# Optimization experiments

Hardware: AMD Instinct MI355X
Metric: run time of the kernel (lower is better)

Reference implementation:

```python
import jax, jax.numpy as jnp
import numpy as np

EPS_DIST = 1e-7  # matches torch: log((d+1)/(d+1e-7))


def _cdist(x, p):
    # x: (B, N, D), p: (P, D) -> (B, N, P) Euclidean distances
    x2 = jnp.sum(x * x, axis=-1, keepdims=True)        # (B, N, 1)
    p2 = jnp.sum(p * p, axis=-1)                       # (P,)
    d2 = x2 + p2[None, None, :] - 2.0 * jnp.einsum('bnd,pd->bnp', x, p)
    return jnp.sqrt(jnp.maximum(d2, 1e-12))


def setup_inputs() -> dict:
    key = jax.random.key(0)
    k1, k2, k3 = jax.random.split(key, 3)
    B, C, H, W = 32, 2048, 14, 14
    num_classes, npc = 200, 10
    P = num_classes * npc
    x = jax.random.normal(k1, (B, C, H, W), dtype=jnp.float32)
    prototypes = jax.random.normal(k2, (1, P, C), dtype=jnp.float32)
    fc_w = jax.random.normal(k3, (num_classes, P), dtype=jnp.float32) * 0.02
    return {"x": x, "prototypes": prototypes, "fc_w": fc_w}


def reference(x, prototypes, fc_w):
    B, C, H, W = x.shape
    feats = x.reshape(B, C, H * W).transpose(0, 2, 1)   # (B, HW, D)
    protos = prototypes[0]                              # (P, D)
    num_classes = fc_w.shape[0]
    npc = protos.shape[0] // num_classes

    distances = _cdist(feats, protos)                   # (B, HW, P)
    similarity = jnp.log((distances + 1.0) / (distances + EPS_DIST))
    max_similarity = jnp.max(similarity, axis=1)        # (B, P)
    min_distances = jnp.min(distances, axis=1)          # (B, P)
    min_distances_per_class = min_distances.reshape(B, num_classes, npc)
    scores = max_similarity @ fc_w.T                    # (B, num_classes)
    return scores, min_distances_per_class
```

## Files before the change

### kernel.cpp

```cpp
#include <hip/hip_runtime.h>

#define INF_BITS 0x7F800000u
#define AS1 __attribute__((address_space(1)))
#define AS3 __attribute__((address_space(3)))

typedef float f32x4 __attribute__((ext_vector_type(4)));
typedef __bf16 bf16x8 __attribute__((ext_vector_type(8)));
typedef unsigned short u16x4 __attribute__((ext_vector_type(4)));
typedef unsigned short u16x8 __attribute__((ext_vector_type(8)));
typedef unsigned int u32x4 __attribute__((ext_vector_type(4)));

static __device__ __forceinline__ unsigned short f2bf(float f) {
  unsigned int u = __float_as_uint(f);
  return (unsigned short)((u + 0x7FFFu + ((u >> 16) & 1u)) >> 16);
}

__global__ __launch_bounds__(256) void k_prep_p(const float* __restrict__ protos,
                                                unsigned short* __restrict__ pT,
                                                float* __restrict__ p2,
                                                unsigned int* __restrict__ outu) {
  const int row = blockIdx.x;
  const int tid = threadIdx.x;
  const int gi = row * 256 + tid;
  if (gi < 64000) outu[6400 + gi] = INF_BITS;
  __shared__ float red[4];
  float s = 0.f;
  u16x8 h = (u16x8){0, 0, 0, 0, 0, 0, 0, 0};
  if (row < 2000) {
    const float* src = protos + (size_t)row * 2048 + tid * 8;
    f32x4 a = *(const f32x4*)src;
    f32x4 c = *(const f32x4*)(src + 4);
    h = (u16x8){f2bf(a.x), f2bf(a.y), f2bf(a.z), f2bf(a.w),
                f2bf(c.x), f2bf(c.y), f2bf(c.z), f2bf(c.w)};
    s = a.x * a.x + a.y * a.y + a.z * a.z + a.w * a.w +
        c.x * c.x + c.y * c.y + c.z * c.z + c.w * c.w;
  }
  *(u16x8*)(pT + (size_t)row * 2048 + tid * 8) = h;
  #pragma unroll
  for (int off = 32; off; off >>= 1) s += __shfl_xor(s, off);
  if ((tid & 63) == 0) red[tid >> 6] = s;
  __syncthreads();
  if (tid == 0) p2[row] = red[0] + red[1] + red[2] + red[3];
}

__global__ __launch_bounds__(256) void k_prep_x(const float* __restrict__ x,
                                                unsigned short* __restrict__ xT,
                                                float* __restrict__ x2p,
                                                float* __restrict__ x2) {
  const int kt = blockIdx.x;
  const int b  = blockIdx.y;
  const int tid = threadIdx.x;
  if (b == 32) {
    u32x4* pad = (u32x4*)(xT + (size_t)6272 * 2048);
    #pragma unroll
    for (int j = tid; j < 1024; j += 256)
      pad[kt * 1024 + j] = (u32x4){0u, 0u, 0u, 0u};
    if (kt == 0 && tid < 128) x2[6272 + tid] = __uint_as_float(INF_BITS);
    return;
  }
  __shared__ unsigned short Ls[64][204];
  const float* src = x + ((size_t)b * 2048 + (size_t)kt * 64) * 196;
  for (int idx = tid; idx < 3136; idx += 256) {
    const int kk = idx / 49, c4 = idx - kk * 49;
    f32x4 v = *(const f32x4*)(src + (size_t)kk * 196 + c4 * 4);
    *(u16x4*)&Ls[kk][c4 * 4] = (u16x4){f2bf(v.x), f2bf(v.y), f2bf(v.z), f2bf(v.w)};
  }
  __syncthreads();
  if (tid < 196) {
    float s = 0.f;
    #pragma unroll
    for (int j = 0; j < 64; ++j) {
      float v = __uint_as_float((unsigned int)Ls[j][tid] << 16);
      s += v * v;
    }
    x2p[kt * 6272 + b * 196 + tid] = s;
  }
  unsigned short* dstb = xT + (size_t)b * 196 * 2048 + kt * 64;
  for (int idx = tid; idx < 1568; idx += 256) {
    const int n = idx >> 3, q = idx & 7;
    const int k0 = q * 8;
    u32x4 v;
    v.x = (unsigned int)Ls[k0 + 0][n] | ((unsigned int)Ls[k0 + 1][n] << 16);
    v.y = (unsigned int)Ls[k0 + 2][n] | ((unsigned int)Ls[k0 + 3][n] << 16);
    v.z = (unsigned int)Ls[k0 + 4][n] | ((unsigned int)Ls[k0 + 5][n] << 16);
    v.w = (unsigned int)Ls[k0 + 6][n] | ((unsigned int)Ls[k0 + 7][n] << 16);
    *(u32x4*)(dstb + (size_t)n * 2048 + k0) = v;
  }
}

__global__ void k_x2r(const float* __restrict__ x2p, float* __restrict__ x2) {
  int i = blockIdx.x * blockDim.x + threadIdx.x;
  if (i >= 6272) return;
  float s = 0.f;
  #pragma unroll
  for (int c = 0; c < 32; ++c) s += x2p[c * 6272 + i];
  x2[i] = s;
}

__global__ __launch_bounds__(512, 2) void k_main(
    const unsigned short* __restrict__ pT, const unsigned short* __restrict__ xT,
    const float* __restrict__ p2, const float* __restrict__ x2,
    unsigned int* __restrict__ outu) {
  const int orig = blockIdx.x;
  const int wgid = (orig & 7) * 25 + (orig >> 3);
  const int ptpair = wgid / 50;
  const int rem = wgid - ptpair * 50;
  const int ptile = ptpair * 2 + (rem & 1);
  const int mtile = rem >> 1;
  const int p0 = ptile * 256;
  const int m0 = mtile * 256;
  const int tid = threadIdx.x;
  const int lane = tid & 63;
  const int w = tid >> 6;
  const int wp = w >> 2;
  const int wn = w & 3;
  const int lr = lane & 15;
  const int lg = lane >> 4;

  __shared__ __align__(16) char S[131072];

  f32x4 acc[8][4];
  #pragma unroll
  for (int mi = 0; mi < 8; ++mi)
    #pragma unroll
    for (int ni = 0; ni < 4; ++ni)
      acc[mi][ni] = (f32x4){0.f, 0.f, 0.f, 0.f};

  const int rowbase = tid >> 3;
  const int chunk = (tid & 7) ^ (rowbase & 7);
  const char* gA = (const char*)pT + (size_t)(p0 + rowbase) * 4096 + chunk * 16;
  const char* gB = (const char*)xT + (size_t)(m0 + rowbase) * 4096 + chunk * 16;
  const int wbase = w * 1024;

#define STAGE_A(c_, kt_, h_) do {                                              \
    const char* s_ = gA + (size_t)((h_) * 128 * 4096) + (size_t)(kt_) * 128;   \
    _Pragma("unroll")                                                          \
    for (int j_ = 0; j_ < 2; ++j_)                                             \
      __builtin_amdgcn_global_load_lds(                                        \
          (const AS1 void*)(s_ + (size_t)j_ * 64 * 4096),                      \
          (AS3 void*)(S + (c_) * 32768 + (h_) * 16384 + j_ * 8192 + wbase),    \
          16, 0, 0);                                                           \
  } while (0)
#define STAGE_B(c_, kt_, h_) do {                                              \
    const char* s_ = gB + (size_t)((h_) * 128 * 4096) + (size_t)(kt_) * 128;   \
    _Pragma("unroll")                                                          \
    for (int j_ = 0; j_ < 2; ++j_)                                             \
      __builtin_amdgcn_global_load_lds(                                        \
          (const AS1 void*)(s_ + (size_t)j_ * 64 * 4096),                      \
          (AS3 void*)(S + 65536 + (c_) * 32768 + (h_) * 16384 + j_ * 8192 + wbase), \
          16, 0, 0);                                                           \
  } while (0)

  const int swz = ((lr & 7) << 4);
  const int arow = (wp * 128 + lr) * 128;
  const int brow = (wn * 64 + lr) * 128;
  const int koff0 = (lg * 16) ^ swz;
  const int koff1 = (64 + lg * 16) ^ swz;

#define READ_A(dst_, c_, ko_, hf_)                                             \
    _Pragma("unroll")                                                          \
    for (int mi_ = 0; mi_ < 4; ++mi_)                                          \
      dst_[mi_] = *(const bf16x8*)(S + (c_) * 32768 + arow + (hf_) * 8192 +    \
                                   mi_ * 2048 + (ko_));
#define READ_B(dst_, c_, ko_)                                                  \
    _Pragma("unroll")                                                          \
    for (int ni_ = 0; ni_ < 4; ++ni_)                                          \
      dst_[ni_] = *(const bf16x8*)(S + 65536 + (c_) * 32768 + brow +           \
                                   ni_ * 2048 + (ko_));

#define PH_BAR() do { __builtin_amdgcn_sched_barrier(0);                       \
    __builtin_amdgcn_s_barrier(); __builtin_amdgcn_sched_barrier(0); } while (0)
#define LGKM0() do { asm volatile("s_waitcnt lgkmcnt(0)" ::: "memory");        \
    __builtin_amdgcn_sched_barrier(0); } while (0)
#define MFMA_Q(mlo_, af_, bf_) do { __builtin_amdgcn_s_setprio(1);             \
    _Pragma("unroll")                                                          \
    for (int mi_ = (mlo_); mi_ < (mlo_) + 4; ++mi_)                            \
      _Pragma("unroll")                                                        \
      for (int ni_ = 0; ni_ < 4; ++ni_)                                        \
        acc[mi_][ni_] = __builtin_amdgcn_mfma_f32_16x16x32_bf16(               \
            af_[mi_ - (mlo_)], bf_[ni_], acc[mi_][ni_], 0, 0, 0);              \
    __builtin_amdgcn_s_setprio(0); } while (0)

#define KT_BODY(kt_, c_, sa_, sb_, vm_) do {                                   \
    bf16x8 alo[4], ahi[4], bk0[4], bk1[4];                                     \
    READ_A(alo, c_, koff0, 0);                                                 \
    READ_B(bk0, c_, koff0);                                                    \
    if (sa_) STAGE_A((c_) ^ 1, (kt_) + 1, 0);                                  \
    PH_BAR(); LGKM0();                                                         \
    MFMA_Q(0, alo, bk0);                                                       \
    PH_BAR();                                                                  \
    READ_A(ahi, c_, koff0, 1);                                                 \
    READ_B(bk1, c_, koff1);                                                    \
    if (sa_) STAGE_A((c_) ^ 1, (kt_) + 1, 1);                                  \
    PH_BAR(); LGKM0();                                                         \
    MFMA_Q(4, ahi, bk0);                                                       \
    PH_BAR();                                                                  \
    READ_A(alo, c_, koff1, 0);                                                 \
    if (sb_) STAGE_B(c_, (kt_) + 2, 0);                                        \
    PH_BAR(); LGKM0();                                                         \
    MFMA_Q(0, alo, bk1);                                                       \
    PH_BAR();                                                                  \
    READ_A(ahi, c_, koff1, 1);                                                 \
    if (sb_) STAGE_B(c_, (kt_) + 2, 1);                                        \
    if ((vm_) == 4)      asm volatile("s_waitcnt vmcnt(4)" ::: "memory");      \
    else if ((vm_) == 0) asm volatile("s_waitcnt vmcnt(0)" ::: "memory");      \
    __builtin_amdgcn_sched_barrier(0);                                         \
    PH_BAR(); LGKM0();                                                         \
    MFMA_Q(4, ahi, bk1);                                                       \
    PH_BAR();                                                                  \
  } while (0)

  STAGE_B(0, 0, 0); STAGE_B(0, 0, 1);
  STAGE_A(0, 0, 0); STAGE_A(0, 0, 1);
  STAGE_B(1, 1, 0); STAGE_B(1, 1, 1);
  asm volatile("s_waitcnt vmcnt(4)" ::: "memory");
  __builtin_amdgcn_sched_barrier(0);
  __builtin_amdgcn_s_barrier();
  __builtin_amdgcn_sched_barrier(0);

  #pragma unroll 1
  for (int it = 0; it < 15; ++it) {
    KT_BODY(2 * it, 0, 1, 1, 4);
    KT_BODY(2 * it + 1, 1, 1, 1, 4);
  }
  KT_BODY(30, 0, 1, 0, 0);
  KT_BODY(31, 1, 0, 0, -1);
#undef KT_BODY
#undef MFMA_Q
#undef READ_A
#undef READ_B
#undef STAGE_A
#undef STAGE_B

  const int wm_base = m0 + wn * 64;
  const int b_lo = wm_base / 196;
  int b_hi = (wm_base + 63) / 196;
  if (b_hi > 31) b_hi = 31;
  const bool wave_ok = (b_lo < 32);
  float x2v[4];
  int seg0[4];
  #pragma unroll
  for (int ni = 0; ni < 4; ++ni) {
    const int m = wm_base + ni * 16 + lr;
    x2v[ni] = x2[m];
    seg0[ni] = ((m / 196) == b_lo);
  }
  const float INF = __uint_as_float(INF_BITS);
  #pragma unroll
  for (int mi = 0; mi < 8; ++mi) {
    const int prow = p0 + wp * 128 + mi * 16 + 4 * lg;
    #pragma unroll
    for (int j = 0; j < 4; ++j) {
      const int p = prow + j;
      const float pp = p2[p];
      float ma = INF, mb = INF;
      #pragma unroll
      for (int ni = 0; ni < 4; ++ni) {
        const float d2 = x2v[ni] + pp - 2.f * acc[mi][ni][j];
        ma = fminf(ma, seg0[ni] ? d2 : INF);
        mb = fminf(mb, seg0[ni] ? INF : d2);
      }
      #pragma unroll
      for (int off = 1; off < 16; off <<= 1) {
        ma = fminf(ma, __shfl_xor(ma, off));
        mb = fminf(mb, __shfl_xor(mb, off));
      }
      if (lr == 0 && p < 2000 && wave_ok) {
        atomicMin(&outu[6400 + b_lo * 2000 + p], __float_as_uint(fmaxf(ma, 0.f)));
        if (b_hi != b_lo)
          atomicMin(&outu[6400 + b_hi * 2000 + p], __float_as_uint(fmaxf(mb, 0.f)));
      }
    }
  }
}

__global__ void k_post(float* __restrict__ out, float* __restrict__ simbuf) {
  int i = blockIdx.x * blockDim.x + threadIdx.x;
  if (i >= 64000) return;
  float d2 = out[6400 + i];
  float d = sqrtf(fmaxf(d2, 1e-12f));
  out[6400 + i] = d;
  simbuf[i] = logf((d + 1.0f) / (d + 1e-7f));
}

__global__ __launch_bounds__(256) void k_scores(const float* __restrict__ fc_w,
                                                const float* __restrict__ simbuf,
                                                float* __restrict__ out) {
  const int id = blockIdx.x * 4 + (threadIdx.x >> 6);
  const int lane = threadIdx.x & 63;
  const int b = id / 200;
  const int c = id - b * 200;
  const f32x4* sv = (const f32x4*)(simbuf + (size_t)b * 2000);
  const f32x4* wv = (const f32x4*)(fc_w + (size_t)c * 2000);
  float s = 0.f;
  #pragma unroll
  for (int it = 0; it < 8; ++it) {
    int i = lane + it * 64;
    if (i < 500) {
      f32x4 a = sv[i], w4 = wv[i];
      s += a.x * w4.x + a.y * w4.y + a.z * w4.z + a.w * w4.w;
    }
  }
  #pragma unroll
  for (int off = 32; off; off >>= 1) s += __shfl_xor(s, off);
  if (lane == 0) out[b * 200 + c] = s;
}

extern "C" void kernel_launch(void* const* d_in, const int* in_sizes, int n_in,
                              void* d_out, int out_size, void* d_ws, size_t ws_size,
                              hipStream_t stream) {
  const float* x      = (const float*)d_in[0];
  const float* protos = (const float*)d_in[1];
  const float* fc_w   = (const float*)d_in[2];
  float* out = (float*)d_out;

  char* wsb = (char*)d_ws;
  unsigned short* pT = (unsigned short*)wsb;
  unsigned short* xT = (unsigned short*)(wsb + 8388608);
  float* p2   = (float*)(wsb + 34603008);
  float* x2   = (float*)(wsb + 34611200);
  float* x2p  = (float*)(wsb + 34636800);
  float* simb = (float*)(wsb + 34636800);

  k_prep_p<<<2048, 256, 0, stream>>>(protos, pT, p2, (unsigned int*)d_out);
  k_prep_x<<<dim3(32, 33), 256, 0, stream>>>(x, xT, x2p, x2);
  k_x2r<<<25, 256, 0, stream>>>(x2p, x2);
  k_main<<<200, 512, 0, stream>>>(pT, xT, p2, x2, (unsigned int*)d_out);
  k_post<<<250, 256, 0, stream>>>(out, simb);
  k_scores<<<1600, 256, 0, stream>>>(fc_w, simb, out);
}
```

Before: 97.35 us.

## Restructure GEMM main loop into register double-buffered full-tile pipeline

Replaces the four-phase per-k-tile schedule, which interleaved partial LDS reads, staged loads and barriers, with a register ping-pong pipeline. Each tile now reads the full A (8) and B (4) fragments for one k-half while the MFMAs for the previous half run, then issues a full stage of the next tile after a vmcnt(0) wait and barrier. This cuts the barrier count per tile from eight to two and aims to overlap LDS reads with MFMA. In exchange it raises register pressure and drains all outstanding global loads every tile, which can expose memory latency.

Measured after the change: 159.1 us. 1.63x slower.

```diff
diff --git a/kernel.cpp b/kernel.cpp
--- a/kernel.cpp
+++ b/kernel.cpp
@@ -150,6 +150,9 @@
           (AS3 void*)(S + 65536 + (c_) * 32768 + (h_) * 16384 + j_ * 8192 + wbase), \
           16, 0, 0);                                                           \
   } while (0)
+#define STAGE_FULL(c_, kt_) do {                                               \
+    STAGE_A(c_, kt_, 0); STAGE_A(c_, kt_, 1);                                  \
+    STAGE_B(c_, kt_, 0); STAGE_B(c_, kt_, 1); } while (0)
 
   const int swz = ((lr & 7) << 4);
   const int arow = (wp * 128 + lr) * 128;
@@ -157,78 +160,88 @@
   const int koff0 = (lg * 16) ^ swz;
   const int koff1 = (64 + lg * 16) ^ swz;
 
-#define READ_A(dst_, c_, ko_, hf_)                                             \
-    _Pragma("unroll")                                                          \
-    for (int mi_ = 0; mi_ < 4; ++mi_)                                          \
-      dst_[mi_] = *(const bf16x8*)(S + (c_) * 32768 + arow + (hf_) * 8192 +    \
-                                   mi_ * 2048 + (ko_));
-#define READ_B(dst_, c_, ko_)                                                  \
+#define READ_A8(dst_, c_, ko_)                                                 \
+    _Pragma("unroll")                                                          \
+    for (int mi_ = 0; mi_ < 8; ++mi_)                                          \
+      dst_[mi_] = *(const bf16x8*)(S + (c_) * 32768 + arow + (mi_ >> 2) * 8192 \
+                                   + (mi_ & 3) * 2048 + (ko_));
+#define READ_B4(dst_, c_, ko_)                                                 \
     _Pragma("unroll")                                                          \
     for (int ni_ = 0; ni_ < 4; ++ni_)                                          \
       dst_[ni_] = *(const bf16x8*)(S + 65536 + (c_) * 32768 + brow +           \
                                    ni_ * 2048 + (ko_));
-
-#define PH_BAR() do { __builtin_amdgcn_sched_barrier(0);                       \
-    __builtin_amdgcn_s_barrier(); __builtin_amdgcn_sched_barrier(0); } while (0)
-#define LGKM0() do { asm volatile("s_waitcnt lgkmcnt(0)" ::: "memory");        \
-    __builtin_amdgcn_sched_barrier(0); } while (0)
-#define MFMA_Q(mlo_, af_, bf_) do { __builtin_amdgcn_s_setprio(1);             \
-    _Pragma("unroll")                                                          \
-    for (int mi_ = (mlo_); mi_ < (mlo_) + 4; ++mi_)                            \
+#define MFMA_SET(xa_, xb_) do { __builtin_amdgcn_s_setprio(1);                 \
+    _Pragma("unroll")                                                          \
+    for (int mi_ = 0; mi_ < 8; ++mi_)                                          \
       _Pragma("unroll")                                                        \
       for (int ni_ = 0; ni_ < 4; ++ni_)                                        \
         acc[mi_][ni_] = __builtin_amdgcn_mfma_f32_16x16x32_bf16(               \
-            af_[mi_ - (mlo_)], bf_[ni_], acc[mi_][ni_], 0, 0, 0);              \
+            xa_[mi_], xb_[ni_], acc[mi_][ni_], 0, 0, 0);                       \
     __builtin_amdgcn_s_setprio(0); } while (0)
 
-#define KT_BODY(kt_, c_, sa_, sb_, vm_) do {                                   \
-    bf16x8 alo[4], ahi[4], bk0[4], bk1[4];                                     \
-    READ_A(alo, c_, koff0, 0);                                                 \
-    READ_B(bk0, c_, koff0);                                                    \
-    if (sa_) STAGE_A((c_) ^ 1, (kt_) + 1, 0);                                  \
-    PH_BAR(); LGKM0();                                                         \
-    MFMA_Q(0, alo, bk0);                                                       \
-    PH_BAR();                                                                  \
-    READ_A(ahi, c_, koff0, 1);                                                 \
-    READ_B(bk1, c_, koff1);                                                    \
-    if (sa_) STAGE_A((c_) ^ 1, (kt_) + 1, 1);                                  \
-    PH_BAR(); LGKM0();                                                         \
-    MFMA_Q(4, ahi, bk0);                                                       \
-    PH_BAR();                                                                  \
-    READ_A(alo, c_, koff1, 0);                                                 \
-    if (sb_) STAGE_B(c_, (kt_) + 2, 0);                                        \
-    PH_BAR(); LGKM0();                                                         \
-    MFMA_Q(0, alo, bk1);                                                       \
-    PH_BAR();                                                                  \
-    READ_A(ahi, c_, koff1, 1);                                                 \
-    if (sb_) STAGE_B(c_, (kt_) + 2, 1);                                        \
-    if ((vm_) == 4)      asm volatile("s_waitcnt vmcnt(4)" ::: "memory");      \
-    else if ((vm_) == 0) asm volatile("s_waitcnt vmcnt(0)" ::: "memory");      \
-    __builtin_amdgcn_sched_barrier(0);                                         \
-    PH_BAR(); LGKM0();                                                         \
-    MFMA_Q(4, ahi, bk1);                                                       \
-    PH_BAR();                                                                  \
+#define SCHED() __builtin_amdgcn_sched_barrier(0)
+#define SBAR() do { SCHED(); __builtin_amdgcn_s_barrier(); SCHED(); } while (0)
+#define LGKM0() do { asm volatile("s_waitcnt lgkmcnt(0)" ::: "memory"); SCHED(); } while (0)
+#define VM0() do { asm volatile("s_waitcnt vmcnt(0)" ::: "memory"); SCHED(); } while (0)
+
+  bf16x8 Aa[8], Ab[4], Ba[8], Bb[4];
+
+  STAGE_FULL(0, 0);
+  STAGE_FULL(1, 1);
+  asm volatile("s_waitcnt vmcnt(8)" ::: "memory");
+  SCHED();
+  __builtin_amdgcn_s_barrier();
+  SCHED();
+
+  READ_A8(Aa, 0, koff0); READ_B4(Ab, 0, koff0);
+  SCHED();
+  READ_A8(Ba, 0, koff1); READ_B4(Bb, 0, koff1);
+  SCHED();
+  MFMA_SET(Aa, Ab);
+  SCHED();
+  LGKM0();
+  SBAR();
+  VM0();
+  STAGE_FULL(0, 2);
+  SBAR();
+
+#define KT_STEADY(kt_, c_, st_) do {                                           \
+    READ_A8(Aa, c_, koff0); READ_B4(Ab, c_, koff0);                            \
+    SCHED();                                                                   \
+    MFMA_SET(Ba, Bb);                    \
+    SCHED();                                                                   \
+    READ_A8(Ba, c_, koff1); READ_B4(Bb, c_, koff1);                            \
+    SCHED();                                                                   \
+    MFMA_SET(Aa, Ab);                    \
+    SCHED();                                                                   \
+    LGKM0();                                     \
+    SBAR();                                                 \
+    VM0();                    \
+    if (st_) STAGE_FULL(c_, (kt_) + 2);                                        \
+    SBAR();                                               \
   } while (0)
 
-  STAGE_B(0, 0, 0); STAGE_B(0, 0, 1);
-  STAGE_A(0, 0, 0); STAGE_A(0, 0, 1);
-  STAGE_B(1, 1, 0); STAGE_B(1, 1, 1);
-  asm volatile("s_waitcnt vmcnt(4)" ::: "memory");
-  __builtin_amdgcn_sched_barrier(0);
-  __builtin_amdgcn_s_barrier();
-  __builtin_amdgcn_sched_barrier(0);
-
   #pragma unroll 1
-  for (int it = 0; it < 15; ++it) {
-    KT_BODY(2 * it, 0, 1, 1, 4);
-    KT_BODY(2 * it + 1, 1, 1, 1, 4);
-  }
-  KT_BODY(30, 0, 1, 0, 0);
-  KT_BODY(31, 1, 0, 0, -1);
-#undef KT_BODY
-#undef MFMA_Q
-#undef READ_A
-#undef READ_B
+  for (int it = 0; it < 14; ++it) {
+    KT_STEADY(2 * it + 1, 1, 1);
+    KT_STEADY(2 * it + 2, 0, 1);
+  }
+  KT_STEADY(29, 1, 1);
+  KT_STEADY(30, 0, 0);
+  READ_A8(Aa, 1, koff0); READ_B4(Ab, 1, koff0);
+  SCHED();
+  MFMA_SET(Ba, Bb);
+  SCHED();
+  READ_A8(Ba, 1, koff1); READ_B4(Bb, 1, koff1);
+  SCHED();
+  MFMA_SET(Aa, Ab);
+  SCHED();
+  MFMA_SET(Ba, Bb);
+#undef KT_STEADY
+#undef MFMA_SET
+#undef READ_A8
+#undef READ_B4
+#undef STAGE_FULL
 #undef STAGE_A
 #undef STAGE_B
 
```

## Switch distance GEMM from bf16 to fp8 operands with fp8 MFMA

Applied to the files above, without the earlier changes.

Quantizes prototypes and features to fp8 instead of bf16 in the prep kernels and computes the squared norms from the dequantized fp8 values so they stay consistent. The main GEMM now uses 16x16x32 fp8 MFMAs, with half-size rows, a new LDS swizzle and 8-byte operand reads, and half as many K-tile iterations. This halves the bytes moved and stored and raises peak matrix throughput. In exchange, fp8 has much lower precision, which may break accuracy tolerance on distances, especially for the min-distance and log-similarity outputs.

New measurement: 99.84 us. +2.6%, slower.

```diff
diff --git a/kernel.cpp b/kernel.cpp
--- a/kernel.cpp
+++ b/kernel.cpp
@@ -5,18 +5,16 @@
 #define AS3 __attribute__((address_space(3)))
 
 typedef float f32x4 __attribute__((ext_vector_type(4)));
-typedef __bf16 bf16x8 __attribute__((ext_vector_type(8)));
-typedef unsigned short u16x4 __attribute__((ext_vector_type(4)));
-typedef unsigned short u16x8 __attribute__((ext_vector_type(8)));
+typedef unsigned int u32x2 __attribute__((ext_vector_type(2)));
 typedef unsigned int u32x4 __attribute__((ext_vector_type(4)));
 
-static __device__ __forceinline__ unsigned short f2bf(float f) {
-  unsigned int u = __float_as_uint(f);
-  return (unsigned short)((u + 0x7FFFu + ((u >> 16) & 1u)) >> 16);
+template <int SEL>
+static __device__ __forceinline__ float dq8(unsigned int w) {
+  return __builtin_amdgcn_cvt_f32_fp8((int)w, SEL);
 }
 
 __global__ __launch_bounds__(256) void k_prep_p(const float* __restrict__ protos,
-                                                unsigned short* __restrict__ pT,
+                                                unsigned char* __restrict__ pTf,
                                                 float* __restrict__ p2,
                                                 unsigned int* __restrict__ outu) {
   const int row = blockIdx.x;
@@ -25,17 +23,26 @@
   if (gi < 64000) outu[6400 + gi] = INF_BITS;
   __shared__ float red[4];
   float s = 0.f;
-  u16x8 h = (u16x8){0, 0, 0, 0, 0, 0, 0, 0};
+  unsigned int w0 = 0u, w1 = 0u;
   if (row < 2000) {
     const float* src = protos + (size_t)row * 2048 + tid * 8;
     f32x4 a = *(const f32x4*)src;
     f32x4 c = *(const f32x4*)(src + 4);
-    h = (u16x8){f2bf(a.x), f2bf(a.y), f2bf(a.z), f2bf(a.w),
-                f2bf(c.x), f2bf(c.y), f2bf(c.z), f2bf(c.w)};
-    s = a.x * a.x + a.y * a.y + a.z * a.z + a.w * a.w +
-        c.x * c.x + c.y * c.y + c.z * c.z + c.w * c.w;
-  }
-  *(u16x8*)(pT + (size_t)row * 2048 + tid * 8) = h;
+    w0 = (unsigned int)__builtin_amdgcn_cvt_pk_fp8_f32(a.x, a.y, 0, false);
+    w0 = (unsigned int)__builtin_amdgcn_cvt_pk_fp8_f32(a.z, a.w, (int)w0, true);
+    w1 = (unsigned int)__builtin_amdgcn_cvt_pk_fp8_f32(c.x, c.y, 0, false);
+    w1 = (unsigned int)__builtin_amdgcn_cvt_pk_fp8_f32(c.z, c.w, (int)w1, true);
+    float q;
+    q = dq8<0>(w0); s += q * q;
+    q = dq8<1>(w0); s += q * q;
+    q = dq8<2>(w0); s += q * q;
+    q = dq8<3>(w0); s += q * q;
+    q = dq8<0>(w1); s += q * q;
+    q = dq8<1>(w1); s += q * q;
+    q = dq8<2>(w1); s += q * q;
+    q = dq8<3>(w1); s += q * q;
+  }
+  *(u32x2*)(pTf + (size_t)row * 2048 + tid * 8) = (u32x2){w0, w1};
   #pragma unroll
   for (int off = 32; off; off >>= 1) s += __shfl_xor(s, off);
   if ((tid & 63) == 0) red[tid >> 6] = s;
@@ -44,46 +51,51 @@
 }
 
 __global__ __launch_bounds__(256) void k_prep_x(const float* __restrict__ x,
-                                                unsigned short* __restrict__ xT,
+                                                unsigned char* __restrict__ xTf,
                                                 float* __restrict__ x2p,
                                                 float* __restrict__ x2) {
   const int kt = blockIdx.x;
   const int b  = blockIdx.y;
   const int tid = threadIdx.x;
   if (b == 32) {
-    u32x4* pad = (u32x4*)(xT + (size_t)6272 * 2048);
-    #pragma unroll
-    for (int j = tid; j < 1024; j += 256)
-      pad[kt * 1024 + j] = (u32x4){0u, 0u, 0u, 0u};
+    u32x4* pad = (u32x4*)(xTf + (size_t)6272 * 2048);
+    #pragma unroll
+    for (int j = tid; j < 512; j += 256)
+      pad[kt * 512 + j] = (u32x4){0u, 0u, 0u, 0u};
     if (kt == 0 && tid < 128) x2[6272 + tid] = __uint_as_float(INF_BITS);
     return;
   }
-  __shared__ unsigned short Ls[64][204];
+  __shared__ unsigned char Ls[64][208];
   const float* src = x + ((size_t)b * 2048 + (size_t)kt * 64) * 196;
   for (int idx = tid; idx < 3136; idx += 256) {
     const int kk = idx / 49, c4 = idx - kk * 49;
     f32x4 v = *(const f32x4*)(src + (size_t)kk * 196 + c4 * 4);
-    *(u16x4*)&Ls[kk][c4 * 4] = (u16x4){f2bf(v.x), f2bf(v.y), f2bf(v.z), f2bf(v.w)};
+    unsigned int w = (unsigned int)__builtin_amdgcn_cvt_pk_fp8_f32(v.x, v.y, 0, false);
+    w = (unsigned int)__builtin_amdgcn_cvt_pk_fp8_f32(v.z, v.w, (int)w, true);
+    *(unsigned int*)&Ls[kk][c4 * 4] = w;
   }
   __syncthreads();
   if (tid < 196) {
     float s = 0.f;
     #pragma unroll
     for (int j = 0; j < 64; ++j) {
-      float v = __uint_as_float((unsigned int)Ls[j][tid] << 16);
+      float v = dq8<0>((unsigned int)Ls[j][tid]);
       s += v * v;
     }
     x2p[kt * 6272 + b * 196 + tid] = s;
   }
-  unsigned short* dstb = xT + (size_t)b * 196 * 2048 + kt * 64;
-  for (int idx = tid; idx < 1568; idx += 256) {
-    const int n = idx >> 3, q = idx & 7;
-    const int k0 = q * 8;
+  unsigned char* dstb = xTf + (size_t)b * 196 * 2048 + kt * 64;
+  for (int idx = tid; idx < 784; idx += 256) {
+    const int n = idx >> 2, q = idx & 3;
+    const int k0 = q * 16;
     u32x4 v;
-    v.x = (unsigned int)Ls[k0 + 0][n] | ((unsigned int)Ls[k0 + 1][n] << 16);
-    v.y = (unsigned int)Ls[k0 + 2][n] | ((unsigned int)Ls[k0 + 3][n] << 16);
-    v.z = (unsigned int)Ls[k0 + 4][n] | ((unsigned int)Ls[k0 + 5][n] << 16);
-    v.w = (unsigned int)Ls[k0 + 6][n] | ((unsigned int)Ls[k0 + 7][n] << 16);
+    #pragma unroll
+    for (int j = 0; j < 4; ++j) {
+      v[j] = (unsigned int)Ls[k0 + 4 * j + 0][n] |
+             ((unsigned int)Ls[k0 + 4 * j + 1][n] << 8) |
+             ((unsigned int)Ls[k0 + 4 * j + 2][n] << 16) |
+             ((unsigned int)Ls[k0 + 4 * j + 3][n] << 24);
+    }
     *(u32x4*)(dstb + (size_t)n * 2048 + k0) = v;
   }
 }
@@ -98,7 +110,7 @@
 }
 
 __global__ __launch_bounds__(512, 2) void k_main(
-    const unsigned short* __restrict__ pT, const unsigned short* __restrict__ xT,
+    const unsigned char* __restrict__ pTf, const unsigned char* __restrict__ xTf,
     const float* __restrict__ p2, const float* __restrict__ x2,
     unsigned int* __restrict__ outu) {
   const int orig = blockIdx.x;
@@ -128,45 +140,50 @@
 
   const int rowbase = tid >> 3;
   const int chunk = (tid & 7) ^ (rowbase & 7);
-  const char* gA = (const char*)pT + (size_t)(p0 + rowbase) * 4096 + chunk * 16;
-  const char* gB = (const char*)xT + (size_t)(m0 + rowbase) * 4096 + chunk * 16;
+  const char* gA = (const char*)pTf + (size_t)(p0 + rowbase) * 2048 + chunk * 16;
+  const char* gB = (const char*)xTf + (size_t)(m0 + rowbase) * 2048 + chunk * 16;
   const int wbase = w * 1024;
 
 #define STAGE_A(c_, kt_, h_) do {                                              \
-    const char* s_ = gA + (size_t)((h_) * 128 * 4096) + (size_t)(kt_) * 128;   \
+    const char* s_ = gA + (size_t)((h_) * 128 * 2048) + (size_t)(kt_) * 128;   \
     _Pragma("unroll")                                                          \
     for (int j_ = 0; j_ < 2; ++j_)                                             \
       __builtin_amdgcn_global_load_lds(                                        \
-          (const AS1 void*)(s_ + (size_t)j_ * 64 * 4096),                      \
+          (const AS1 void*)(s_ + (size_t)j_ * 64 * 2048),                      \
           (AS3 void*)(S + (c_) * 32768 + (h_) * 16384 + j_ * 8192 + wbase),    \
           16, 0, 0);                                                           \
   } while (0)
 #define STAGE_B(c_, kt_, h_) do {                                              \
-    const char* s_ = gB + (size_t)((h_) * 128 * 4096) + (size_t)(kt_) * 128;   \
+    const char* s_ = gB + (size_t)((h_) * 128 * 2048) + (size_t)(kt_) * 128;   \
     _Pragma("unroll")                                                          \
     for (int j_ = 0; j_ < 2; ++j_)                                             \
       __builtin_amdgcn_global_load_lds(                                        \
-          (const AS1 void*)(s_ + (size_t)j_ * 64 * 4096),                      \
+          (const AS1 void*)(s_ + (size_t)j_ * 64 * 2048),                      \
           (AS3 void*)(S + 65536 + (c_) * 32768 + (h_) * 16384 + j_ * 8192 + wbase), \
           16, 0, 0);                                                           \
   } while (0)
 
-  const int swz = ((lr & 7) << 4);
   const int arow = (wp * 128 + lr) * 128;
   const int brow = (wn * 64 + lr) * 128;
-  const int koff0 = (lg * 16) ^ swz;
-  const int koff1 = (64 + lg * 16) ^ swz;
-
-#define READ_A(dst_, c_, ko_, hf_)                                             \
-    _Pragma("unroll")                                                          \
-    for (int mi_ = 0; mi_ < 4; ++mi_)                                          \
-      dst_[mi_] = *(const bf16x8*)(S + (c_) * 32768 + arow + (hf_) * 8192 +    \
-                                   mi_ * 2048 + (ko_));
-#define READ_B(dst_, c_, ko_)                                                  \
-    _Pragma("unroll")                                                          \
-    for (int ni_ = 0; ni_ < 4; ++ni_)                                          \
-      dst_[ni_] = *(const bf16x8*)(S + 65536 + (c_) * 32768 + brow +           \
-                                   ni_ * 2048 + (ko_));
+  int koff[4];
+  #pragma unroll
+  for (int ks = 0; ks < 4; ++ks)
+    koff[ks] = (((2 * ks + (lg >> 1)) ^ (lr & 7)) << 4) | ((lg & 1) << 3);
+
+#define READ_A(dst_, c_, hf_, kp_)                                             \
+    _Pragma("unroll")                                                          \
+    for (int ks_ = 0; ks_ < 2; ++ks_)                                          \
+      _Pragma("unroll")                                                        \
+      for (int mi_ = 0; mi_ < 4; ++mi_)                                        \
+        dst_[ks_ * 4 + mi_] = *(const long*)(S + (c_) * 32768 + arow +         \
+            ((hf_) * 4 + mi_) * 2048 + koff[(kp_) * 2 + ks_]);
+#define READ_B(dst_, c_, kp_)                                                  \
+    _Pragma("unroll")                                                          \
+    for (int ks_ = 0; ks_ < 2; ++ks_)                                          \
+      _Pragma("unroll")                                                        \
+      for (int ni_ = 0; ni_ < 4; ++ni_)                                        \
+        dst_[ks_ * 4 + ni_] = *(const long*)(S + 65536 + (c_) * 32768 + brow + \
+            ni_ * 2048 + koff[(kp_) * 2 + ks_]);
 
 #define PH_BAR() do { __builtin_amdgcn_sched_barrier(0);                       \
     __builtin_amdgcn_s_barrier(); __builtin_amdgcn_sched_barrier(0); } while (0)
@@ -174,39 +191,42 @@
     __builtin_amdgcn_sched_barrier(0); } while (0)
 #define MFMA_Q(mlo_, af_, bf_) do { __builtin_amdgcn_s_setprio(1);             \
     _Pragma("unroll")                                                          \
-    for (int mi_ = (mlo_); mi_ < (mlo_) + 4; ++mi_)                            \
+    for (int ks_ = 0; ks_ < 2; ++ks_)                                          \
       _Pragma("unroll")                                                        \
-      for (int ni_ = 0; ni_ < 4; ++ni_)                                        \
-        acc[mi_][ni_] = __builtin_amdgcn_mfma_f32_16x16x32_bf16(               \
-            af_[mi_ - (mlo_)], bf_[ni_], acc[mi_][ni_], 0, 0, 0);              \
+      for (int mi_ = 0; mi_ < 4; ++mi_)                                        \
+        _Pragma("unroll")                                                      \
+        for (int ni_ = 0; ni_ < 4; ++ni_)                                      \
+          acc[(mlo_) + mi_][ni_] = __builtin_amdgcn_mfma_f32_16x16x32_fp8_fp8( \
+              af_[ks_ * 4 + mi_], bf_[ks_ * 4 + ni_], acc[(mlo_) + mi_][ni_],  \
+              0, 0, 0);                                                        \
     __builtin_amdgcn_s_setprio(0); } while (0)
 
 #define KT_BODY(kt_, c_, sa_, sb_, vm_) do {                                   \
-    bf16x8 alo[4], ahi[4], bk0[4], bk1[4];                                     \
-    READ_A(alo, c_, koff0, 0);                                                 \
-    READ_B(bk0, c_, koff0);                                                    \
+    long alo[8], ahi[8], b01[8], b23[8];                                       \
+    READ_A(alo, c_, 0, 0);                                                     \
+    READ_B(b01, c_, 0);                                                        \
     if (sa_) STAGE_A((c_) ^ 1, (kt_) + 1, 0);                                  \
     PH_BAR(); LGKM0();                                                         \
-    MFMA_Q(0, alo, bk0);                                                       \
+    MFMA_Q(0, alo, b01);                                                       \
     PH_BAR();                                                                  \
-    READ_A(ahi, c_, koff0, 1);                                                 \
-    READ_B(bk1, c_, koff1);                                                    \
+    READ_A(ahi, c_, 1, 0);                                                     \
+    READ_B(b23, c_, 1);                                                        \
     if (sa_) STAGE_A((c_) ^ 1, (kt_) + 1, 1);                                  \
     PH_BAR(); LGKM0();                                                         \
-    MFMA_Q(4, ahi, bk0);                                                       \
+    MFMA_Q(4, ahi, b01);                                                       \
     PH_BAR();                                                                  \
-    READ_A(alo, c_, koff1, 0);                                                 \
+    READ_A(alo, c_, 0, 1);                                                     \
     if (sb_) STAGE_B(c_, (kt_) + 2, 0);                                        \
     PH_BAR(); LGKM0();                                                         \
-    MFMA_Q(0, alo, bk1);                                                       \
+    MFMA_Q(0, alo, b23);                                                       \
     PH_BAR();                                                                  \
-    READ_A(ahi, c_, koff1, 1);                                                 \
+    READ_A(ahi, c_, 1, 1);                                                     \
     if (sb_) STAGE_B(c_, (kt_) + 2, 1);                                        \
     if ((vm_) == 4)      asm volatile("s_waitcnt vmcnt(4)" ::: "memory");      \
     else if ((vm_) == 0) asm volatile("s_waitcnt vmcnt(0)" ::: "memory");      \
     __builtin_amdgcn_sched_barrier(0);                                         \
     PH_BAR(); LGKM0();                                                         \
-    MFMA_Q(4, ahi, bk1);                                                       \
+    MFMA_Q(4, ahi, b23);                                                       \
     PH_BAR();                                                                  \
   } while (0)
 
@@ -219,12 +239,12 @@
   __builtin_amdgcn_sched_barrier(0);
 
   #pragma unroll 1
-  for (int it = 0; it < 15; ++it) {
+  for (int it = 0; it < 7; ++it) {
     KT_BODY(2 * it, 0, 1, 1, 4);
     KT_BODY(2 * it + 1, 1, 1, 1, 4);
   }
-  KT_BODY(30, 0, 1, 0, 0);
-  KT_BODY(31, 1, 0, 0, -1);
+  KT_BODY(14, 0, 1, 0, 0);
+  KT_BODY(15, 1, 0, 0, -1);
 #undef KT_BODY
 #undef MFMA_Q
 #undef READ_A
@@ -315,17 +335,17 @@
   float* out = (float*)d_out;
 
   char* wsb = (char*)d_ws;
-  unsigned short* pT = (unsigned short*)wsb;
-  unsigned short* xT = (unsigned short*)(wsb + 8388608);
-  float* p2   = (float*)(wsb + 34603008);
-  float* x2   = (float*)(wsb + 34611200);
-  float* x2p  = (float*)(wsb + 34636800);
-  float* simb = (float*)(wsb + 34636800);
-
-  k_prep_p<<<2048, 256, 0, stream>>>(protos, pT, p2, (unsigned int*)d_out);
-  k_prep_x<<<dim3(32, 33), 256, 0, stream>>>(x, xT, x2p, x2);
+  unsigned char* pTf = (unsigned char*)wsb;
+  unsigned char* xTf = (unsigned char*)(wsb + 4194304);
+  float* p2   = (float*)(wsb + 17301504);
+  float* x2   = (float*)(wsb + 17309696);
+  float* x2p  = (float*)(wsb + 17335296);
+  float* simb = (float*)(wsb + 17335296);
+
+  k_prep_p<<<2048, 256, 0, stream>>>(protos, pTf, p2, (unsigned int*)d_out);
+  k_prep_x<<<dim3(32, 33), 256, 0, stream>>>(x, xTf, x2p, x2);
   k_x2r<<<25, 256, 0, stream>>>(x2p, x2);
-  k_main<<<200, 512, 0, stream>>>(pT, xT, p2, x2, (unsigned int*)d_out);
+  k_main<<<200, 512, 0, stream>>>(pTf, xTf, p2, x2, (unsigned int*)d_out);
   k_post<<<250, 256, 0, stream>>>(out, simb);
   k_scores<<<1600, 256, 0, stream>>>(fc_w, simb, out);
 }
```
